# Optimization experiments

Measured on AMD Instinct MI355X. Metric: run time of the kernel, lower is better.

The kernel has to match this reference:

```python
import jax, jax.numpy as jnp
import numpy as np

NUM_CLASSES = 80
REG_MAX = 16
CLS_W, BOX_W, DFL_W = 1.0, 2.5, 0.5


def _make_anchors(img=640, strides=(8, 16, 32)):
    pts, strs = [], []
    for s in strides:
        n = img // s
        xs = (np.arange(n, dtype=np.float32) + 0.5) * s
        gy, gx = np.meshgrid(xs, xs, indexing='ij')
        pts.append(np.stack([gx.ravel(), gy.ravel()], axis=1))
        strs.append(np.full((n * n, 1), float(s), np.float32))
    return np.concatenate(pts, 0).astype(np.float32), np.concatenate(strs, 0)


def setup_inputs() -> dict:
    key = jax.random.key(0)
    k1, k2, k3, k4, k5 = jax.random.split(key, 5)
    B, G = 16, 20
    ap, st = _make_anchors()  # A = 8400
    A = ap.shape[0]
    cls_scores = jax.random.uniform(k1, (B, A, NUM_CLASSES), dtype=jnp.float32)
    reg_distri = jax.random.normal(k2, (B, A, 4 * (REG_MAX + 1)), dtype=jnp.float32)
    cxcy = jax.random.uniform(k3, (B, G, 2), dtype=jnp.float32) * 560.0 + 40.0
    wh = jax.random.uniform(k4, (B, G, 2), dtype=jnp.float32) * 120.0 + 20.0
    gt_boxes = jnp.concatenate([cxcy - wh * 0.5, cxcy + wh * 0.5], axis=-1)  # xyxy
    gt_labels = jax.random.randint(k5, (B, G), 0, NUM_CLASSES)
    return {"cls_scores": cls_scores, "reg_distri": reg_distri, "gt_boxes": gt_boxes,
            "anchor_points": jnp.asarray(ap), "stride_tensor": jnp.asarray(st),
            "gt_labels": gt_labels}


def _per_image(pred_cls, pred_reg, gt_boxes, gt_labels, anchor_points, stride):
    A, C = pred_cls.shape
    G = gt_boxes.shape[0]
    k = max(min(13, A // max(G, 1)), 3)
    p = jnp.clip(pred_cls, 1e-7, 1.0 - 1e-7)
    centers = (gt_boxes[:, :2] + gt_boxes[:, 2:]) * 0.5                    # [G,2]
    d = jnp.sqrt(jnp.sum((anchor_points[:, None, :] - centers[None]) ** 2, -1))  # [A,G]
    _, topk_idx = jax.lax.top_k(-d.T, k)                                    # [G,k] nearest anchors
    ax = anchor_points[topk_idx]                                            # [G,k,2]
    inside = ((ax[..., 0] >= gt_boxes[:, None, 0]) & (ax[..., 0] <= gt_boxes[:, None, 2]) &
              (ax[..., 1] >= gt_boxes[:, None, 1]) & (ax[..., 1] <= gt_boxes[:, None, 3]))
    any_in = inside.any(-1, keepdims=True)
    assign_k = jnp.where(any_in, inside, jnp.arange(k) < 3)                 # fallback: 3 nearest
    assign = jnp.zeros((G, A), bool).at[jnp.arange(G)[:, None], topk_idx].set(assign_k)
    aT = assign.T                                                           # [A,G]
    fg = aT.any(1)                                                          # [A]
    last_gt = (G - 1) - jnp.argmax(aT[:, ::-1], axis=1)
    target_box = jnp.where(fg[:, None], gt_boxes[last_gt], 0.0)             # [A,4]
    onehot = jax.nn.one_hot(gt_labels, C, dtype=p.dtype)                    # [G,C]
    target_cls = jnp.max(aT[:, :, None].astype(p.dtype) * onehot[None], axis=1)  # [A,C]
    bce = -(target_cls * jnp.log(p) + (1.0 - target_cls) * jnp.log(1.0 - p))
    num_pos = fg.sum().astype(p.dtype)
    pos_w = jnp.minimum(A / jnp.maximum(num_pos, 1.0), 50.0)
    fgf = fg.astype(p.dtype)[:, None]
    pos_loss = jnp.where(num_pos > 0,
                         jnp.sum(bce * fgf) / jnp.maximum(num_pos * C, 1.0) * pos_w, 0.0)
    neg_loss = jnp.sum(bce * (1.0 - fgf)) / jnp.maximum((A - num_pos) * C, 1.0)
    # box decode (DFL expectation) + smooth-L1 on fg anchors
    reg = jax.nn.softmax(pred_reg.reshape(A, 4, REG_MAX + 1), axis=-1)
    proj = jnp.arange(REG_MAX + 1, dtype=p.dtype)
    dist = jnp.sum(reg * proj, axis=-1)                                     # [A,4]
    s = stride[:, 0]
    pb = jnp.stack([anchor_points[:, 0] - dist[:, 0] * s,
                    anchor_points[:, 1] - dist[:, 1] * s,
                    anchor_points[:, 0] + dist[:, 2] * s,
                    anchor_points[:, 1] + dist[:, 3] * s], axis=-1)
    diff = pb - target_box
    ad = jnp.abs(diff)
    sl1 = jnp.where(ad < 1.0, 0.5 * diff * diff, ad - 0.5)
    box_loss = jnp.where(num_pos > 0,
                         jnp.sum(sl1 * fgf) / jnp.maximum(num_pos * 4.0, 1.0), 0.0)
    return pos_loss + neg_loss, box_loss


def reference(cls_scores, reg_distri, gt_boxes, anchor_points, stride_tensor, gt_labels):
    cls_l, box_l = jax.vmap(
        lambda pc, pr, gb, gl: _per_image(pc, pr, gb, gl, anchor_points, stride_tensor)
    )(cls_scores, reg_distri, gt_boxes, gt_labels)
    loss_cls = cls_l.mean() * CLS_W
    loss_box = box_l.mean() * BOX_W
    return loss_cls + loss_box  # loss_dfl is identically 0 in the original
```

## Files before the change

kernel.cpp:

```cpp
#include <hip/hip_runtime.h>
#include <hip/hip_bf16.h>
#include <cfloat>

#define C_NUM 80
#define REG_MAXP1 17
#define NS 33
#define MAXA 8448
#define FG_STRIDE 512

__device__ inline void cand_for_slot(int sc, float cx, float cy, float& v, int& idx)
{
    v = FLT_MAX; idx = 0x7fffffff;
    int loc, w, n, strd, base;
    if (sc < 36)      { loc = sc;      w = 6; n = 80; strd = 8;  base = 0; }
    else if (sc < 52) { loc = sc - 36; w = 4; n = 40; strd = 16; base = 6400; }
    else if (sc < 68) { loc = sc - 52; w = 4; n = 20; strd = 32; base = 8000; }
    else return;
    float inv = 1.0f / (float)strd;
    int ix0 = (int)floorf(cx * inv - 0.5f) - (w / 2 - 1);
    int iy0 = (int)floorf(cy * inv - 0.5f) - (w / 2 - 1);
    int ix = ix0 + loc % w, iy = iy0 + loc / w;
    if (ix < 0 || ix >= n || iy < 0 || iy >= n) return;
    float ax = ((float)ix + 0.5f) * (float)strd;
    float ay = ((float)iy + 0.5f) * (float)strd;
    float dx = ax - cx, dy = ay - cy;
    v = dx * dx + dy * dy;
    idx = base + iy * n + ix;
}

__global__ __launch_bounds__(64) void assign_fast_kernel(const float* __restrict__ gt_boxes,
                              int* __restrict__ sel,
                              int G, int k)
{
    int bg = blockIdx.x;
    int b = bg / G, g = bg % G;
    const float* box = gt_boxes + (size_t)(b * G + g) * 4;
    float x0 = box[0], y0 = box[1], x1 = box[2], y1 = box[3];
    float cx = (x0 + x1) * 0.5f, cy = (y0 + y1) * 0.5f;
    int lane = threadIdx.x;

    float v0, v1; int i0, i1;
    cand_for_slot(lane,      cx, cy, v0, i0);
    cand_for_slot(lane + 64, cx, cy, v1, i1);

    int my_sel = 0x7fffffff;
    for (int it = 0; it < k; ++it) {
        float lb; int li; bool s0;
        if (v0 < v1 || (v0 == v1 && i0 < i1)) { lb = v0; li = i0; s0 = true; }
        else                                   { lb = v1; li = i1; s0 = false; }
        float rb = lb; int ri = li;
        for (int off = 32; off; off >>= 1) {
            float ov = __shfl_down(rb, off);
            int   oi = __shfl_down(ri, off);
            if (ov < rb || (ov == rb && oi < ri)) { rb = ov; ri = oi; }
        }
        int win = __shfl(ri, 0);
        if (lane == it) my_sel = win;
        if (li == win) {
            if (s0) { v0 = FLT_MAX; i0 = 0x7fffffff; }
            else    { v1 = FLT_MAX; i1 = 0x7fffffff; }
        }
    }

    bool inside = false;
    if (lane < k && my_sel < 0x7fffffff) {
        int idx = my_sel, n, strd, base;
        if (idx < 6400)      { n = 80; strd = 8;  base = 0; }
        else if (idx < 8000) { n = 40; strd = 16; base = 6400; }
        else                 { n = 20; strd = 32; base = 8000; }
        int loc = idx - base;
        float ax = ((float)(loc % n) + 0.5f) * (float)strd;
        float ay = ((float)(loc / n) + 0.5f) * (float)strd;
        inside = (ax >= x0) && (ax <= x1) && (ay >= y0) && (ay <= y1);
    }
    unsigned long long ball = __ballot(inside);
    if (lane < 16) {
        int out = -1;
        if (lane < k && my_sel < 0x7fffffff) {
            bool asg = ball ? inside : (lane < 3);
            out = asg ? my_sel : -1;
        }
        sel[(size_t)bg * 16 + lane] = out;
    }
}

__global__ __launch_bounds__(256) void assign_kernel(const float* __restrict__ gt_boxes,
                              const float* __restrict__ anchor_points,
                              int* __restrict__ sel,
                              int B, int A, int G, int k)
{
    __shared__ float s_val[4];
    __shared__ int   s_idx[4];
    __shared__ int   s_sel;
    __shared__ int   s_topk[16];
    __shared__ int   s_anyin;

    int bg = blockIdx.x;
    int b = bg / G, g = bg % G;
    const float* box = gt_boxes + (size_t)(b * G + g) * 4;
    float x0 = box[0], y0 = box[1], x1 = box[2], y1 = box[3];
    float cx = (x0 + x1) * 0.5f, cy = (y0 + y1) * 0.5f;

    int t = threadIdx.x;
    float dv[NS];
#pragma unroll
    for (int s = 0; s < NS; ++s) {
        int i = t + s * 256;
        float d = FLT_MAX;
        if (i < A) {
            float dx = anchor_points[2 * i] - cx;
            float dy = anchor_points[2 * i + 1] - cy;
            d = dx * dx + dy * dy;
        }
        dv[s] = d;
    }

    int wid = t >> 6, lane = t & 63;
    for (int it = 0; it < k; ++it) {
        float best = FLT_MAX; int bi = 0x7fffffff;
#pragma unroll
        for (int s = 0; s < NS; ++s) {
            if (dv[s] < best) { best = dv[s]; bi = t + s * 256; }
        }
        for (int off = 32; off; off >>= 1) {
            float ov = __shfl_down(best, off);
            int   oi = __shfl_down(bi, off);
            if (ov < best || (ov == best && oi < bi)) { best = ov; bi = oi; }
        }
        if (lane == 0) { s_val[wid] = best; s_idx[wid] = bi; }
        __syncthreads();
        if (t == 0) {
            float bv = s_val[0]; int bix = s_idx[0];
#pragma unroll
            for (int w = 1; w < 4; ++w) {
                if (s_val[w] < bv || (s_val[w] == bv && s_idx[w] < bix)) { bv = s_val[w]; bix = s_idx[w]; }
            }
            s_sel = bix;
            s_topk[it] = bix;
        }
        __syncthreads();
        int selx = s_sel;
        if ((selx & 255) == t) {
            int slot = selx >> 8;
#pragma unroll
            for (int s = 0; s < NS; ++s) if (s == slot) dv[s] = FLT_MAX;
        }
    }

    if (t == 0) s_anyin = 0;
    __syncthreads();
    bool inside = false; int aidx = -1;
    if (t < k) {
        aidx = s_topk[t];
        float ax = anchor_points[2 * aidx], ay = anchor_points[2 * aidx + 1];
        inside = (ax >= x0) && (ax <= x1) && (ay >= y0) && (ay <= y1);
        if (inside) atomicOr(&s_anyin, 1);
    }
    __syncthreads();
    if (t < k) {
        bool asg = s_anyin ? inside : (t < 3);
        sel[(size_t)bg * 16 + t] = asg ? aidx : -1;
    }
}

__global__ __launch_bounds__(256) void raster_kernel(const int* __restrict__ sel,
                              unsigned int* __restrict__ mask,
                              int* __restrict__ fglist,
                              int* __restrict__ npos,
                              float* __restrict__ acc,
                              int A, int G, int k)
{
    __shared__ unsigned int lmask[MAXA];
    __shared__ int s_cnt;
    int b = blockIdx.x, t = threadIdx.x;

    for (int i = t; i < A; i += 256) lmask[i] = 0u;
    if (t == 0) s_cnt = 0;
    if (t < 3) acc[b * 3 + t] = 0.f;
    __syncthreads();

    for (int i = t; i < G * 16; i += 256) {
        int slot = i & 15;
        if (slot < k) {
            int a = sel[(size_t)(b * G) * 16 + i];
            if (a >= 0) atomicOr(&lmask[a], 1u << (i >> 4));
        }
    }
    __syncthreads();

    for (int i = t; i < A; i += 256) {
        unsigned int m = lmask[i];
        mask[(size_t)b * A + i] = m;
        if (m) {
            int lg = 31 - __clz(m);
            int p = atomicAdd(&s_cnt, 1);
            fglist[b * FG_STRIDE + p] = i | (lg << 16);
        }
    }
    __syncthreads();
    if (t == 0) npos[b] = s_cnt;
}

__global__ __launch_bounds__(256) void cls_kernel(const float4* __restrict__ cls,
                           const unsigned int* __restrict__ mask,
                           const int* __restrict__ gt_labels,
                           float* __restrict__ acc, int A, int G)
{
    const int CQ = C_NUM / 4;
    int b = blockIdx.y;
    int nq = A * CQ;
    const float4* base = cls + (size_t)b * nq;
    const unsigned int* mrow = mask + (size_t)b * A;
    const int* lab = gt_labels + (size_t)b * G;

    float pos = 0.f, neg = 0.f;
    for (int q = blockIdx.x * 256 + threadIdx.x; q < nq; q += gridDim.x * 256) {
        float4 v = base[q];
        unsigned int m = mrow[q / CQ];
        float p0 = fminf(fmaxf(v.x, 1e-7f), 1.0f - 1e-7f);
        float p1 = fminf(fmaxf(v.y, 1e-7f), 1.0f - 1e-7f);
        float p2 = fminf(fmaxf(v.z, 1e-7f), 1.0f - 1e-7f);
        float p3 = fminf(fmaxf(v.w, 1e-7f), 1.0f - 1e-7f);
        if (m) {
            int c0 = (q % CQ) * 4;
            unsigned int tm = 0, mm = m;
            while (mm) {
                int g = __ffs(mm) - 1;
                mm &= mm - 1;
                unsigned int d = (unsigned int)(lab[g] - c0);
                if (d < 4u) tm |= 1u << d;
            }
            pos -= __logf((tm & 1u) ? p0 : 1.0f - p0);
            pos -= __logf((tm & 2u) ? p1 : 1.0f - p1);
            pos -= __logf((tm & 4u) ? p2 : 1.0f - p2);
            pos -= __logf((tm & 8u) ? p3 : 1.0f - p3);
        } else {
            neg -= __logf(1.0f - p0) + __logf(1.0f - p1) + __logf(1.0f - p2) + __logf(1.0f - p3);
        }
    }

    for (int off = 32; off; off >>= 1) {
        pos += __shfl_down(pos, off);
        neg += __shfl_down(neg, off);
    }
    __shared__ float sp[4], sn[4];
    int wid = threadIdx.x >> 6, lane = threadIdx.x & 63;
    if (lane == 0) { sp[wid] = pos; sn[wid] = neg; }
    __syncthreads();
    if (threadIdx.x == 0) {
        float P = sp[0] + sp[1] + sp[2] + sp[3];
        float N = sn[0] + sn[1] + sn[2] + sn[3];
        if (P != 0.f) atomicAdd(&acc[b * 3 + 0], P);
        if (N != 0.f) atomicAdd(&acc[b * 3 + 1], N);
    }
}

__global__ __launch_bounds__(256) void boxfg_kernel(const float* __restrict__ reg,
                           const float* __restrict__ gt_boxes,
                           const float* __restrict__ ap,
                           const float* __restrict__ st,
                           const int* __restrict__ fglist,
                           const int* __restrict__ npos,
                           float* __restrict__ acc, int A, int G)
{
    int b = blockIdx.y;
    int e = blockIdx.x * 256 + threadIdx.x;
    float bx = 0.f;
    if (e < npos[b]) {
        int ent = fglist[b * FG_STRIDE + e];
        int a = ent & 0xffff;
        int lg = ent >> 16;
        const float* tb = gt_boxes + (size_t)(b * G + lg) * 4;
        const float* r = reg + ((size_t)b * A + a) * (4 * REG_MAXP1);
        float s = st[a];
        float axp = ap[2 * a], ayp = ap[2 * a + 1];
#pragma unroll
        for (int j = 0; j < 4; ++j) {
            const float* rj = r + j * REG_MAXP1;
            float rr[REG_MAXP1];
#pragma unroll
            for (int i = 0; i < REG_MAXP1; ++i) rr[i] = rj[i];
            float mx = rr[0];
#pragma unroll
            for (int i = 1; i < REG_MAXP1; ++i) mx = fmaxf(mx, rr[i]);
            float sum = 0.f, dot = 0.f;
#pragma unroll
            for (int i = 0; i < REG_MAXP1; ++i) {
                float ev = __expf(rr[i] - mx);
                sum += ev; dot += ev * (float)i;
            }
            float dist = dot / sum;
            float pbj = (j < 2) ? ((j == 0 ? axp : ayp) - dist * s)
                                : ((j == 2 ? axp : ayp) + dist * s);
            float df = pbj - tb[j];
            float ad = fabsf(df);
            bx += (ad < 1.0f) ? 0.5f * df * df : ad - 0.5f;
        }
    }
    for (int off = 32; off; off >>= 1) bx += __shfl_down(bx, off);
    __shared__ float sb[4];
    int wid = threadIdx.x >> 6, lane = threadIdx.x & 63;
    if (lane == 0) sb[wid] = bx;
    __syncthreads();
    if (threadIdx.x == 0) {
        float X = sb[0] + sb[1] + sb[2] + sb[3];
        if (X != 0.f) atomicAdd(&acc[b * 3 + 2], X);
    }
}

__global__ void final_kernel(const float* __restrict__ acc,
                             const int* __restrict__ npos,
                             float* __restrict__ out, int B, int A)
{
    if (threadIdx.x == 0 && blockIdx.x == 0) {
        float cls_sum = 0.f, box_sum = 0.f;
        for (int b = 0; b < B; ++b) {
            float np = (float)npos[b];
            float neg = acc[b * 3 + 1] / fmaxf(((float)A - np) * (float)C_NUM, 1.0f);
            float pos = 0.f, box = 0.f;
            if (np > 0.f) {
                float pw = fminf((float)A / fmaxf(np, 1.0f), 50.0f);
                pos = acc[b * 3 + 0] / fmaxf(np * (float)C_NUM, 1.0f) * pw;
                box = acc[b * 3 + 2] / fmaxf(np * 4.0f, 1.0f);
            }
            cls_sum += pos + neg;
            box_sum += box;
        }
        out[0] = cls_sum / (float)B * 1.0f + box_sum / (float)B * 2.5f;
    }
}

extern "C" void kernel_launch(void* const* d_in, const int* in_sizes, int n_in,
                              void* d_out, int out_size, void* d_ws, size_t ws_size,
                              hipStream_t stream)
{
    const float* cls   = (const float*)d_in[0];
    const float* reg   = (const float*)d_in[1];
    const float* gtb   = (const float*)d_in[2];
    const float* ap    = (const float*)d_in[3];
    const float* st    = (const float*)d_in[4];
    const int*   glab  = (const int*)d_in[5];

    int A = in_sizes[3] / 2;
    int B = in_sizes[0] / (A * C_NUM);
    int G = in_sizes[5] / B;
    int k = A / (G > 1 ? G : 1); if (k > 13) k = 13; if (k < 3) k = 3;

    unsigned int* mask = (unsigned int*)d_ws;
    float* acc   = (float*)(mask + (size_t)B * A);
    int*   npos  = (int*)(acc + 3 * B);
    int*   sel   = npos + B;
    int*   fgl   = sel + (size_t)B * G * 16;

    if (A == 8400) {
        assign_fast_kernel<<<B * G, 64, 0, stream>>>(gtb, sel, G, k);
    } else {
        assign_kernel<<<B * G, 256, 0, stream>>>(gtb, ap, sel, B, A, G, k);
    }

    raster_kernel<<<B, 256, 0, stream>>>(sel, mask, fgl, npos, acc, A, G, k);

    dim3 g3(128, B);
    cls_kernel<<<g3, 256, 0, stream>>>((const float4*)cls, mask, glab, acc, A, G);

    dim3 g4((FG_STRIDE + 255) / 256, B);
    boxfg_kernel<<<g4, 256, 0, stream>>>(reg, gtb, ap, st, fgl, npos, acc, A, G);

    final_kernel<<<1, 64, 0, stream>>>(acc, npos, (float*)d_out, B, A);
}
```

Before: 153.9 us.

## Fuse anchor assignment with rasterization and fold box loss into cls kernel

Merges the per-GT assignment kernel and the per-image raster kernel into one 1024-thread block per image, where each wavefront handles one GT and writes assignment bits straight into a shared mask, with a ballot-based foreground list append. Separately, the box smooth-L1 loss computation moves into the classification kernel's first blocks, sharing its reduction and removing a launch. This cuts two kernel launches and the intermediate sel buffer round-trip. In exchange, the 1024-thread block needs about 33KB of shared memory, and only B blocks run for the assignment stage.

Measured after the change: 159.9 us. 3.9% more time.

```diff
diff --git a/kernel.cpp b/kernel.cpp
--- a/kernel.cpp
+++ b/kernel.cpp
@@ -28,60 +28,86 @@
     idx = base + iy * n + ix;
 }
 
-__global__ __launch_bounds__(64) void assign_fast_kernel(const float* __restrict__ gt_boxes,
-                              int* __restrict__ sel,
-                              int G, int k)
-{
-    int bg = blockIdx.x;
-    int b = bg / G, g = bg % G;
-    const float* box = gt_boxes + (size_t)(b * G + g) * 4;
-    float x0 = box[0], y0 = box[1], x1 = box[2], y1 = box[3];
-    float cx = (x0 + x1) * 0.5f, cy = (y0 + y1) * 0.5f;
-    int lane = threadIdx.x;
-
-    float v0, v1; int i0, i1;
-    cand_for_slot(lane,      cx, cy, v0, i0);
-    cand_for_slot(lane + 64, cx, cy, v1, i1);
-
-    int my_sel = 0x7fffffff;
-    for (int it = 0; it < k; ++it) {
-        float lb; int li; bool s0;
-        if (v0 < v1 || (v0 == v1 && i0 < i1)) { lb = v0; li = i0; s0 = true; }
-        else                                   { lb = v1; li = i1; s0 = false; }
-        float rb = lb; int ri = li;
-        for (int off = 32; off; off >>= 1) {
-            float ov = __shfl_down(rb, off);
-            int   oi = __shfl_down(ri, off);
-            if (ov < rb || (ov == rb && oi < ri)) { rb = ov; ri = oi; }
-        }
-        int win = __shfl(ri, 0);
-        if (lane == it) my_sel = win;
-        if (li == win) {
-            if (s0) { v0 = FLT_MAX; i0 = 0x7fffffff; }
-            else    { v1 = FLT_MAX; i1 = 0x7fffffff; }
-        }
-    }
-
-    bool inside = false;
-    if (lane < k && my_sel < 0x7fffffff) {
-        int idx = my_sel, n, strd, base;
-        if (idx < 6400)      { n = 80; strd = 8;  base = 0; }
-        else if (idx < 8000) { n = 40; strd = 16; base = 6400; }
-        else                 { n = 20; strd = 32; base = 8000; }
-        int loc = idx - base;
-        float ax = ((float)(loc % n) + 0.5f) * (float)strd;
-        float ay = ((float)(loc / n) + 0.5f) * (float)strd;
-        inside = (ax >= x0) && (ax <= x1) && (ay >= y0) && (ay <= y1);
-    }
-    unsigned long long ball = __ballot(inside);
-    if (lane < 16) {
-        int out = -1;
+__global__ __launch_bounds__(1024) void assignraster_kernel(const float* __restrict__ gt_boxes,
+                              unsigned int* __restrict__ mask,
+                              int* __restrict__ fglist,
+                              int* __restrict__ npos,
+                              float* __restrict__ acc,
+                              int A, int G, int k)
+{
+    __shared__ unsigned int lmask[8400];
+    __shared__ int s_cnt;
+    int b = blockIdx.x, t = threadIdx.x;
+    int wv = t >> 6, lane = t & 63;
+
+    for (int i = t; i < A; i += 1024) lmask[i] = 0u;
+    if (t == 0) s_cnt = 0;
+    if (t < 3) acc[b * 3 + t] = 0.f;
+    __syncthreads();
+
+    for (int g = wv; g < G; g += 16) {
+        const float* box = gt_boxes + (size_t)(b * G + g) * 4;
+        float x0 = box[0], y0 = box[1], x1 = box[2], y1 = box[3];
+        float cx = (x0 + x1) * 0.5f, cy = (y0 + y1) * 0.5f;
+
+        float v0, v1; int i0, i1;
+        cand_for_slot(lane,      cx, cy, v0, i0);
+        cand_for_slot(lane + 64, cx, cy, v1, i1);
+
+        int my_sel = 0x7fffffff;
+        for (int it = 0; it < k; ++it) {
+            float lb; int li; bool s0;
+            if (v0 < v1 || (v0 == v1 && i0 < i1)) { lb = v0; li = i0; s0 = true; }
+            else                                   { lb = v1; li = i1; s0 = false; }
+            float rb = lb; int ri = li;
+            for (int off = 32; off; off >>= 1) {
+                float ov = __shfl_down(rb, off);
+                int   oi = __shfl_down(ri, off);
+                if (ov < rb || (ov == rb && oi < ri)) { rb = ov; ri = oi; }
+            }
+            int win = __shfl(ri, 0);
+            if (lane == it) my_sel = win;
+            if (li == win) {
+                if (s0) { v0 = FLT_MAX; i0 = 0x7fffffff; }
+                else    { v1 = FLT_MAX; i1 = 0x7fffffff; }
+            }
+        }
+
+        bool inside = false;
+        if (lane < k && my_sel < 0x7fffffff) {
+            int idx = my_sel, n, strd, base;
+            if (idx < 6400)      { n = 80; strd = 8;  base = 0; }
+            else if (idx < 8000) { n = 40; strd = 16; base = 6400; }
+            else                 { n = 20; strd = 32; base = 8000; }
+            int loc = idx - base;
+            float ax = ((float)(loc % n) + 0.5f) * (float)strd;
+            float ay = ((float)(loc / n) + 0.5f) * (float)strd;
+            inside = (ax >= x0) && (ax <= x1) && (ay >= y0) && (ay <= y1);
+        }
+        unsigned long long ball = __ballot(inside);
         if (lane < k && my_sel < 0x7fffffff) {
             bool asg = ball ? inside : (lane < 3);
-            out = asg ? my_sel : -1;
-        }
-        sel[(size_t)bg * 16 + lane] = out;
-    }
+            if (asg) atomicOr(&lmask[my_sel], 1u << g);
+        }
+    }
+    __syncthreads();
+
+    for (int i = t; i < A; i += 1024) {
+        unsigned int m = lmask[i];
+        mask[(size_t)b * A + i] = m;
+        bool fg = (m != 0u);
+        unsigned long long bal = __ballot(fg);
+        int cnt = __popcll(bal);
+        int base = 0;
+        if (lane == 0 && cnt) base = atomicAdd(&s_cnt, cnt);
+        base = __shfl(base, 0);
+        if (fg) {
+            int pre = __popcll(bal & ((1ull << lane) - 1ull));
+            fglist[b * FG_STRIDE + base + pre] = i | ((31 - __clz(m)) << 16);
+        }
+    }
+    __syncthreads();
+    if (t == 0) npos[b] = s_cnt;
 }
 
 __global__ __launch_bounds__(256) void assign_kernel(const float* __restrict__ gt_boxes,
@@ -201,9 +227,15 @@
     if (t == 0) npos[b] = s_cnt;
 }
 
-__global__ __launch_bounds__(256) void cls_kernel(const float4* __restrict__ cls,
+__global__ __launch_bounds__(256) void clsbox_kernel(const float4* __restrict__ cls,
+                           const float* __restrict__ reg,
+                           const float* __restrict__ gt_boxes,
+                           const float* __restrict__ ap,
+                           const float* __restrict__ st,
                            const unsigned int* __restrict__ mask,
                            const int* __restrict__ gt_labels,
+                           const int* __restrict__ fglist,
+                           const int* __restrict__ npos,
                            float* __restrict__ acc, int A, int G)
 {
     const int CQ = C_NUM / 4;
@@ -239,33 +271,8 @@
         }
     }
 
-    for (int off = 32; off; off >>= 1) {
-        pos += __shfl_down(pos, off);
-        neg += __shfl_down(neg, off);
-    }
-    __shared__ float sp[4], sn[4];
-    int wid = threadIdx.x >> 6, lane = threadIdx.x & 63;
-    if (lane == 0) { sp[wid] = pos; sn[wid] = neg; }
-    __syncthreads();
-    if (threadIdx.x == 0) {
-        float P = sp[0] + sp[1] + sp[2] + sp[3];
-        float N = sn[0] + sn[1] + sn[2] + sn[3];
-        if (P != 0.f) atomicAdd(&acc[b * 3 + 0], P);
-        if (N != 0.f) atomicAdd(&acc[b * 3 + 1], N);
-    }
-}
-
-__global__ __launch_bounds__(256) void boxfg_kernel(const float* __restrict__ reg,
-                           const float* __restrict__ gt_boxes,
-                           const float* __restrict__ ap,
-                           const float* __restrict__ st,
-                           const int* __restrict__ fglist,
-                           const int* __restrict__ npos,
-                           float* __restrict__ acc, int A, int G)
-{
-    int b = blockIdx.y;
+    float bx = 0.f;
     int e = blockIdx.x * 256 + threadIdx.x;
-    float bx = 0.f;
     if (e < npos[b]) {
         int ent = fglist[b * FG_STRIDE + e];
         int a = ent & 0xffff;
@@ -297,13 +304,22 @@
             bx += (ad < 1.0f) ? 0.5f * df * df : ad - 0.5f;
         }
     }
-    for (int off = 32; off; off >>= 1) bx += __shfl_down(bx, off);
-    __shared__ float sb[4];
+
+    for (int off = 32; off; off >>= 1) {
+        pos += __shfl_down(pos, off);
+        neg += __shfl_down(neg, off);
+        bx  += __shfl_down(bx, off);
+    }
+    __shared__ float sp[4], sn[4], sb[4];
     int wid = threadIdx.x >> 6, lane = threadIdx.x & 63;
-    if (lane == 0) sb[wid] = bx;
+    if (lane == 0) { sp[wid] = pos; sn[wid] = neg; sb[wid] = bx; }
     __syncthreads();
     if (threadIdx.x == 0) {
+        float P = sp[0] + sp[1] + sp[2] + sp[3];
+        float N = sn[0] + sn[1] + sn[2] + sn[3];
         float X = sb[0] + sb[1] + sb[2] + sb[3];
+        if (P != 0.f) atomicAdd(&acc[b * 3 + 0], P);
+        if (N != 0.f) atomicAdd(&acc[b * 3 + 1], N);
         if (X != 0.f) atomicAdd(&acc[b * 3 + 2], X);
     }
 }
@@ -352,19 +368,16 @@
     int*   sel   = npos + B;
     int*   fgl   = sel + (size_t)B * G * 16;
 
-    if (A == 8400) {
-        assign_fast_kernel<<<B * G, 64, 0, stream>>>(gtb, sel, G, k);
+    if (A == 8400 && G <= 32) {
+        assignraster_kernel<<<B, 1024, 0, stream>>>(gtb, mask, fgl, npos, acc, A, G, k);
     } else {
         assign_kernel<<<B * G, 256, 0, stream>>>(gtb, ap, sel, B, A, G, k);
-    }
-
-    raster_kernel<<<B, 256, 0, stream>>>(sel, mask, fgl, npos, acc, A, G, k);
+        raster_kernel<<<B, 256, 0, stream>>>(sel, mask, fgl, npos, acc, A, G, k);
+    }
 
     dim3 g3(128, B);
-    cls_kernel<<<g3, 256, 0, stream>>>((const float4*)cls, mask, glab, acc, A, G);
-
-    dim3 g4((FG_STRIDE + 255) / 256, B);
-    boxfg_kernel<<<g4, 256, 0, stream>>>(reg, gtb, ap, st, fgl, npos, acc, A, G);
+    clsbox_kernel<<<g3, 256, 0, stream>>>((const float4*)cls, reg, gtb, ap, st,
+                                          mask, glab, fgl, npos, acc, A, G);
 
     final_kernel<<<1, 64, 0, stream>>>(acc, npos, (float*)d_out, B, A);
 }
```
